# Kernel optimization log

Hardware: AMD Instinct MI355X
Metric: run time of the kernel (lower is better)

## Reference

```python
import jax, jax.numpy as jnp
import numpy as np

B, E, S, H = 8, 1024, 2048, 16  # batch, embed_dim, seq_len, n_heads
D = E // H                       # per-head hidden dim


def setup_inputs() -> dict:
    key = jax.random.key(0)
    k1, k2 = jax.random.split(key)
    x = jax.random.normal(k1, (B, E, S), dtype=jnp.float32)
    weight = jax.random.normal(k2, (H, S), dtype=jnp.float32)  # nn.Parameter(torch.randn)
    bias = jnp.zeros((H, S), dtype=jnp.float32)                # nn.Parameter(torch.zeros)
    return {"x": x, "weight": weight, "bias": bias}


def _vector_to_matrix(v):
    # v: (H, S) -> M: (H, S, S), M[h, i, j] = v[h, j - i] if j >= i else 0
    h, m = v.shape
    i = jnp.arange(m)[:, None]
    j = jnp.arange(m)[None, :]
    off = j - i  # negative offsets wrap (same as torch fancy indexing) but are masked out
    return jnp.where(j >= i, v[:, off], jnp.zeros((), dtype=v.dtype))


def reference(x, weight, bias):
    b, e, s = x.shape
    h = weight.shape[0]
    d = e // h
    M = _vector_to_matrix(weight)  # (H, S, S)
    # Original: x.view(B,H,D,S).reshape(B*H,D,S) paired with W.repeat_interleave(B,0),
    # i.e. flat index k uses M[k // B]. Group the flat B*H axis into H contiguous
    # blocks of size B so each block shares one Toeplitz matrix (no (B*H,S,S) blowup).
    xg = x.reshape(b * h, d, s).reshape(h, b, d, s)  # block m = M[m]
    out = jnp.einsum('mbds,mst->mbdt', xg, M) + bias[:, None, None, :]
    return out.reshape(b, e, s)
```

## Files before the change

### kernel.cpp

```cpp
#include <hip/hip_runtime.h>
#include <hip/hip_bf16.h>

#define SEQ    2048
#define NHEAD  16
#define RPH    512
#define BM     128
#define BK     64
#define NTH    256

#define WSTRIDE 2184
#define ABUF_E  8192
#define WCOP_E  (2 * ABUF_E)
#define TOT_E   (WCOP_E + 8 * WSTRIDE)

typedef float  f32x4  __attribute__((ext_vector_type(4)));
typedef __bf16 bf16x8 __attribute__((ext_vector_type(8)));

struct PF { float4 v0, v1, v2, v3, v4, v5, v6, v7; };

__device__ __forceinline__ unsigned f2bf(float f) {
    union { __hip_bfloat16 h; unsigned short u; } cv;
    cv.h = __float2bfloat16(f);
    return (unsigned)cv.u;
}

__device__ __forceinline__ uint4 pack8u(float4 a, float4 b) {
    union { bf16x8 v; uint4 u; } r;
    r.v[0] = (__bf16)a.x; r.v[1] = (__bf16)a.y;
    r.v[2] = (__bf16)a.z; r.v[3] = (__bf16)a.w;
    r.v[4] = (__bf16)b.x; r.v[5] = (__bf16)b.y;
    r.v[6] = (__bf16)b.z; r.v[7] = (__bf16)b.w;
    return r.u;
}

#define MFMA16(a, b, c) __builtin_amdgcn_mfma_f32_16x16x32_bf16((a), (b), (c), 0, 0, 0)

#define LOADPF(P, CH)                                                         \
  { const float* g_ = Xp + (size_t)(CH) * BK;                                 \
    P.v0 = *(const float4*)g_;                                                \
    P.v1 = *(const float4*)(g_ + 4);                                          \
    P.v2 = *(const float4*)(g_ + 8 * SEQ);                                    \
    P.v3 = *(const float4*)(g_ + 8 * SEQ + 4);                                \
    P.v4 = *(const float4*)(g_ + 16 * SEQ);                                   \
    P.v5 = *(const float4*)(g_ + 16 * SEQ + 4);                               \
    P.v6 = *(const float4*)(g_ + 24 * SEQ);                                   \
    P.v7 = *(const float4*)(g_ + 24 * SEQ + 4); }

#define WRITEA(AB, P)                                                         \
  { *(uint4*)((AB) + wb0) = pack8u(P.v0, P.v1);                               \
    *(uint4*)((AB) + wb1) = pack8u(P.v2, P.v3);                               \
    *(uint4*)((AB) + wb2) = pack8u(P.v4, P.v5);                               \
    *(uint4*)((AB) + wb3) = pack8u(P.v6, P.v7); }

#define WINLOAD4(CH, OFFE, S0, S1, S2, S3)                                    \
  { const unsigned short* bq_ = wcB + 64 * (CH) + (OFFE);                     \
    bw[S0] = *(const bf16x8*)(bq_);                                           \
    bw[S1] = *(const bf16x8*)(bq_ + 16);                                      \
    bw[S2] = *(const bf16x8*)(bq_ + 32);                                      \
    bw[S3] = *(const bf16x8*)(bq_ + 48); }

#define KSTEPW(ABC, KS, P8, BASE)                                             \
  { const int kb_ = (64 * (KS) + kq16) ^ swz;                                 \
    bf16x8 af0 = *(const bf16x8*)((ABC) + Arow0 + kb_);                       \
    bf16x8 af1 = *(const bf16x8*)((ABC) + Arow1 + kb_);                       \
    acc[0][0] = MFMA16(af0, bw[((P8)+(BASE)-0)&15], acc[0][0]);               \
    acc[1][0] = MFMA16(af1, bw[((P8)+(BASE)-0)&15], acc[1][0]);               \
    acc[0][1] = MFMA16(af0, bw[((P8)+(BASE)-1)&15], acc[0][1]);               \
    acc[1][1] = MFMA16(af1, bw[((P8)+(BASE)-1)&15], acc[1][1]);               \
    acc[0][2] = MFMA16(af0, bw[((P8)+(BASE)-2)&15], acc[0][2]);               \
    acc[1][2] = MFMA16(af1, bw[((P8)+(BASE)-2)&15], acc[1][2]);               \
    acc[0][3] = MFMA16(af0, bw[((P8)+(BASE)-3)&15], acc[0][3]);               \
    acc[1][3] = MFMA16(af1, bw[((P8)+(BASE)-3)&15], acc[1][3]);               \
    acc[0][4] = MFMA16(af0, bw[((P8)+(BASE)-4)&15], acc[0][4]);               \
    acc[1][4] = MFMA16(af1, bw[((P8)+(BASE)-4)&15], acc[1][4]);               \
    acc[0][5] = MFMA16(af0, bw[((P8)+(BASE)-5)&15], acc[0][5]);               \
    acc[1][5] = MFMA16(af1, bw[((P8)+(BASE)-5)&15], acc[1][5]);               \
    acc[0][6] = MFMA16(af0, bw[((P8)+(BASE)-6)&15], acc[0][6]);               \
    acc[1][6] = MFMA16(af1, bw[((P8)+(BASE)-6)&15], acc[1][6]);               \
    acc[0][7] = MFMA16(af0, bw[((P8)+(BASE)-7)&15], acc[0][7]);               \
    acc[1][7] = MFMA16(af1, bw[((P8)+(BASE)-7)&15], acc[1][7]); }

#define PAIRBODY(P8)                                                          \
  {                                                                           \
    if (ch + 2 < nch) LOADPF(pfA, ch + 2);                                    \
    WRITEA(ab1, pfB);                                                         \
    __builtin_amdgcn_s_setprio(1);                                            \
    KSTEPW(ab0, 0, P8, 7);                                                    \
    KSTEPW(ab0, 1, P8, 9);                                                    \
    __builtin_amdgcn_s_setprio(0);                                            \
    if (ch + 2 < nch)                                                         \
        WINLOAD4(ch, 112, ((P8)+14)&15, ((P8)+15)&15,                         \
                 ((P8)+16)&15, ((P8)+17)&15);                                 \
    if (ch + 3 < nch) LOADPF(pfB, ch + 3);                                    \
    if (ch + 2 < nch) WRITEA(ab0, pfA);                                       \
    __builtin_amdgcn_s_setprio(1);                                            \
    KSTEPW(ab1, 0, P8, 11);                                                   \
    KSTEPW(ab1, 1, P8, 13);                                                   \
    __builtin_amdgcn_s_setprio(0);                                            \
    if (ch + 2 < nch)                                                         \
        WINLOAD4(ch, 176, ((P8)+18)&15, ((P8)+19)&15,                         \
                 ((P8)+20)&15, ((P8)+21)&15);                                 \
  }

__global__ __launch_bounds__(NTH, 2) void mixer_kernel(
    const float* __restrict__ x, const float* __restrict__ wgt,
    const float* __restrict__ bias, float* __restrict__ out)
{
    __shared__ unsigned short smem[TOT_E] __attribute__((aligned(16)));
    char* ab0 = (char*)smem;
    char* ab1 = (char*)smem + ABUF_E * 2;
    unsigned short* wc = smem + WCOP_E;

    const int tid  = threadIdx.x;
    const int lane = tid & 63;
    const int wv   = tid >> 6;

    const int bid  = blockIdx.x;
    const int m    = (bid & 7) + 8 * ((bid >> 3) & 1);
    const int rt   = (bid >> 4) & 3;
    const int pr   = bid >> 6;
    const int ct_hi = 15 - pr;
    const int ct_lo = pr;

    const float* Xb = x   + (size_t)(m * RPH + rt * BM) * SEQ;
    float*       Ob = out + (size_t)(m * RPH + rt * BM) * SEQ;
    const float* wr = wgt  + m * SEQ;
    const float* br = bias + m * SEQ;

    const int sr    = lane >> 3;
    const int sc    = (lane & 7) * 8;
    const int wsw   = ((lane & 7) * 16) ^ (sr << 4);
    const int rbw   = 32 * wv;
    const int wb0   = (rbw + sr)      * 128 + wsw;
    const int wb1   = (rbw + sr + 8)  * 128 + wsw;
    const int wb2   = (rbw + sr + 16) * 128 + wsw;
    const int wb3   = (rbw + sr + 24) * 128 + wsw;
    const float* Xp = Xb + (size_t)(rbw + sr) * SEQ + sc;

    PF pfA, pfB;
    LOADPF(pfA, 0);
    LOADPF(pfB, 1);

    {
        const int t8 = tid * 8;
        const float* g = wr + (2040 - t8);
        float4 lo = *(const float4*)g;
        float4 hi = *(const float4*)(g + 4);
        uint4 v;
        v.x = f2bf(hi.w) | (f2bf(hi.z) << 16);
        v.y = f2bf(hi.y) | (f2bf(hi.x) << 16);
        v.z = f2bf(lo.w) | (f2bf(lo.z) << 16);
        v.w = f2bf(lo.y) | (f2bf(lo.x) << 16);
        *(uint4*)(smem + 8 + t8) = v;
        if (tid < 21) {
            uint4 z = {0u, 0u, 0u, 0u};
            unsigned short* dst = (tid == 0) ? smem
                                 : smem + 8 + 2048 + (tid - 1) * 8;
            *(uint4*)dst = z;
        }
    }
    __syncthreads();

    #pragma unroll
    for (int c = 0; c < 8; ++c) {
        for (int grp = tid; grp < WSTRIDE / 8; grp += NTH) {
            const int i = grp * 8;
            uint4 g0 = *(const uint4*)(smem + 8 + i - 8);
            uint4 g1 = *(const uint4*)(smem + 8 + i);
            unsigned d[9] = {g0.x, g0.y, g0.z, g0.w,
                             g1.x, g1.y, g1.z, g1.w, 0u};
            const int qd = (16 - 2 * c) >> 2;
            uint4 o;
            if (c & 1) {
                o.x = (d[qd]     >> 16) | (d[qd + 1] << 16);
                o.y = (d[qd + 1] >> 16) | (d[qd + 2] << 16);
                o.z = (d[qd + 2] >> 16) | (d[qd + 3] << 16);
                o.w = (d[qd + 3] >> 16) | (d[qd + 4] << 16);
            } else {
                o.x = d[qd];     o.y = d[qd + 1];
                o.z = d[qd + 2]; o.w = d[qd + 3];
            }
            *(uint4*)(wc + c * WSTRIDE + i) = o;
        }
    }
    __syncthreads();

    const int col_low = lane & 15;
    const int kq      = lane >> 4;
    const int kq16    = kq * 16;
    const int swz     = (col_low & 7) << 4;
    const int cpy     = (col_low + 1) & 7;
    const int BcBase  = cpy * WSTRIDE + cpy + 2047 - col_low + 8 * kq;
    const int Arow0   = (rbw      + col_low) * 128;
    const int Arow1   = (rbw + 16 + col_low) * 128;

    #pragma unroll
    for (int half = 0; half < 2; ++half) {
        const int ct  = half ? ct_lo : ct_hi;
        const int t0  = ct << 7;
        const int nch = 2 * (ct + 1);
        const unsigned short* wcB = wc + (BcBase - t0);

        if (half) { LOADPF(pfA, 0); LOADPF(pfB, 1); }
        WRITEA(ab0, pfA);

        bf16x8 bw[16];
        {
            const unsigned short* bq_ = wcB - 112;
            #pragma unroll
            for (int i = 0; i < 14; ++i)
                bw[i] = *(const bf16x8*)(bq_ + 16 * i);
        }

        f32x4 acc[2][8] = {};
        int ch = 0;
        for (;;) {
            PAIRBODY(0);
            ch += 2; if (ch >= nch) break;
            PAIRBODY(8);
            ch += 2; if (ch >= nch) break;
        }

        #pragma unroll
        for (int c = 0; c < 8; ++c) {
            const int colg = t0 + 16 * c + col_low;
            const float bv = br[colg];
            #pragma unroll
            for (int a = 0; a < 2; ++a) {
                const int rowl = rbw + 16 * a + 4 * kq;
                #pragma unroll
                for (int r = 0; r < 4; ++r)
                    Ob[(size_t)(rowl + r) * SEQ + colg] = acc[a][c][r] + bv;
            }
        }
    }
}

extern "C" void kernel_launch(void* const* d_in, const int* in_sizes, int n_in,
                              void* d_out, int out_size, void* d_ws, size_t ws_size,
                              hipStream_t stream) {
    const float* x  = (const float*)d_in[0];
    const float* w  = (const float*)d_in[1];
    const float* bs = (const float*)d_in[2];
    float* out = (float*)d_out;
    dim3 grid(512);
    dim3 block(NTH);
    hipLaunchKernelGGL(mixer_kernel, grid, block, 0, stream, x, w, bs, out);
}
```

Measured before the change: 46.07 us.

## Halve row tile and launch one column tile per block on a larger grid

```diff
diff --git a/kernel.cpp b/kernel.cpp
--- a/kernel.cpp
+++ b/kernel.cpp
@@ -4,19 +4,19 @@
 #define SEQ    2048
 #define NHEAD  16
 #define RPH    512
-#define BM     128
+#define BM     64
 #define BK     64
 #define NTH    256
 
 #define WSTRIDE 2184
-#define ABUF_E  8192
+#define ABUF_E  4096
 #define WCOP_E  (2 * ABUF_E)
 #define TOT_E   (WCOP_E + 8 * WSTRIDE)
 
 typedef float  f32x4  __attribute__((ext_vector_type(4)));
 typedef __bf16 bf16x8 __attribute__((ext_vector_type(8)));
 
-struct PF { float4 v0, v1, v2, v3, v4, v5, v6, v7; };
+struct PF { float4 v0, v1, v2, v3; };
 
 __device__ __forceinline__ unsigned f2bf(float f) {
     union { __hip_bfloat16 h; unsigned short u; } cv;
@@ -39,18 +39,12 @@
   { const float* g_ = Xp + (size_t)(CH) * BK;                                 \
     P.v0 = *(const float4*)g_;                                                \
     P.v1 = *(const float4*)(g_ + 4);                                          \
-    P.v2 = *(const float4*)(g_ + 8 * SEQ);                                    \
-    P.v3 = *(const float4*)(g_ + 8 * SEQ + 4);                                \
-    P.v4 = *(const float4*)(g_ + 16 * SEQ);                                   \
-    P.v5 = *(const float4*)(g_ + 16 * SEQ + 4);                               \
-    P.v6 = *(const float4*)(g_ + 24 * SEQ);                                   \
-    P.v7 = *(const float4*)(g_ + 24 * SEQ + 4); }
+    P.v2 = *(const float4*)(g_ + 8);                                          \
+    P.v3 = *(const float4*)(g_ + 12); }
 
 #define WRITEA(AB, P)                                                         \
   { *(uint4*)((AB) + wb0) = pack8u(P.v0, P.v1);                               \
-    *(uint4*)((AB) + wb1) = pack8u(P.v2, P.v3);                               \
-    *(uint4*)((AB) + wb2) = pack8u(P.v4, P.v5);                               \
-    *(uint4*)((AB) + wb3) = pack8u(P.v6, P.v7); }
+    *(uint4*)((AB) + wb1) = pack8u(P.v2, P.v3); }
 
 #define WINLOAD4(CH, OFFE, S0, S1, S2, S3)                                    \
   { const unsigned short* bq_ = wcB + 64 * (CH) + (OFFE);                     \
@@ -62,23 +56,14 @@
 #define KSTEPW(ABC, KS, P8, BASE)                                             \
   { const int kb_ = (64 * (KS) + kq16) ^ swz;                                 \
     bf16x8 af0 = *(const bf16x8*)((ABC) + Arow0 + kb_);                       \
-    bf16x8 af1 = *(const bf16x8*)((ABC) + Arow1 + kb_);                       \
-    acc[0][0] = MFMA16(af0, bw[((P8)+(BASE)-0)&15], acc[0][0]);               \
-    acc[1][0] = MFMA16(af1, bw[((P8)+(BASE)-0)&15], acc[1][0]);               \
-    acc[0][1] = MFMA16(af0, bw[((P8)+(BASE)-1)&15], acc[0][1]);               \
-    acc[1][1] = MFMA16(af1, bw[((P8)+(BASE)-1)&15], acc[1][1]);               \
-    acc[0][2] = MFMA16(af0, bw[((P8)+(BASE)-2)&15], acc[0][2]);               \
-    acc[1][2] = MFMA16(af1, bw[((P8)+(BASE)-2)&15], acc[1][2]);               \
-    acc[0][3] = MFMA16(af0, bw[((P8)+(BASE)-3)&15], acc[0][3]);               \
-    acc[1][3] = MFMA16(af1, bw[((P8)+(BASE)-3)&15], acc[1][3]);               \
-    acc[0][4] = MFMA16(af0, bw[((P8)+(BASE)-4)&15], acc[0][4]);               \
-    acc[1][4] = MFMA16(af1, bw[((P8)+(BASE)-4)&15], acc[1][4]);               \
-    acc[0][5] = MFMA16(af0, bw[((P8)+(BASE)-5)&15], acc[0][5]);               \
-    acc[1][5] = MFMA16(af1, bw[((P8)+(BASE)-5)&15], acc[1][5]);               \
-    acc[0][6] = MFMA16(af0, bw[((P8)+(BASE)-6)&15], acc[0][6]);               \
-    acc[1][6] = MFMA16(af1, bw[((P8)+(BASE)-6)&15], acc[1][6]);               \
-    acc[0][7] = MFMA16(af0, bw[((P8)+(BASE)-7)&15], acc[0][7]);               \
-    acc[1][7] = MFMA16(af1, bw[((P8)+(BASE)-7)&15], acc[1][7]); }
+    acc[0] = MFMA16(af0, bw[((P8)+(BASE)-0)&15], acc[0]);                     \
+    acc[1] = MFMA16(af0, bw[((P8)+(BASE)-1)&15], acc[1]);                     \
+    acc[2] = MFMA16(af0, bw[((P8)+(BASE)-2)&15], acc[2]);                     \
+    acc[3] = MFMA16(af0, bw[((P8)+(BASE)-3)&15], acc[3]);                     \
+    acc[4] = MFMA16(af0, bw[((P8)+(BASE)-4)&15], acc[4]);                     \
+    acc[5] = MFMA16(af0, bw[((P8)+(BASE)-5)&15], acc[5]);                     \
+    acc[6] = MFMA16(af0, bw[((P8)+(BASE)-6)&15], acc[6]);                     \
+    acc[7] = MFMA16(af0, bw[((P8)+(BASE)-7)&15], acc[7]); }
 
 #define PAIRBODY(P8)                                                          \
   {                                                                           \
@@ -102,7 +87,7 @@
                  ((P8)+20)&15, ((P8)+21)&15);                                 \
   }
 
-__global__ __launch_bounds__(NTH, 2) void mixer_kernel(
+__global__ __launch_bounds__(NTH, 3) void mixer_kernel(
     const float* __restrict__ x, const float* __restrict__ wgt,
     const float* __restrict__ bias, float* __restrict__ out)
 {
@@ -117,25 +102,22 @@
 
     const int bid  = blockIdx.x;
     const int m    = (bid & 7) + 8 * ((bid >> 3) & 1);
-    const int rt   = (bid >> 4) & 3;
-    const int pr   = bid >> 6;
-    const int ct_hi = 15 - pr;
-    const int ct_lo = pr;
+    const int rt   = (bid >> 4) & 7;
+    const int ct   = 15 - (bid >> 7);
+    const int t0   = ct << 7;
+    const int nch  = 2 * (ct + 1);
 
     const float* Xb = x   + (size_t)(m * RPH + rt * BM) * SEQ;
     float*       Ob = out + (size_t)(m * RPH + rt * BM) * SEQ;
     const float* wr = wgt  + m * SEQ;
     const float* br = bias + m * SEQ;
 
-    const int sr    = lane >> 3;
-    const int sc    = (lane & 7) * 8;
-    const int wsw   = ((lane & 7) * 16) ^ (sr << 4);
-    const int rbw   = 32 * wv;
-    const int wb0   = (rbw + sr)      * 128 + wsw;
-    const int wb1   = (rbw + sr + 8)  * 128 + wsw;
-    const int wb2   = (rbw + sr + 16) * 128 + wsw;
-    const int wb3   = (rbw + sr + 24) * 128 + wsw;
-    const float* Xp = Xb + (size_t)(rbw + sr) * SEQ + sc;
+    const int sr    = lane >> 2;
+    const int scq   = lane & 3;
+    const int rbw   = 16 * wv;
+    const int wb0   = (rbw + sr) * 128 + ((scq * 32) ^ ((sr & 7) << 4));
+    const int wb1   = (rbw + sr) * 128 + ((scq * 32 + 16) ^ ((sr & 7) << 4));
+    const float* Xp = Xb + (size_t)(rbw + sr) * SEQ + scq * 16;
 
     PF pfA, pfB;
     LOADPF(pfA, 0);
@@ -191,48 +173,36 @@
     const int swz     = (col_low & 7) << 4;
     const int cpy     = (col_low + 1) & 7;
     const int BcBase  = cpy * WSTRIDE + cpy + 2047 - col_low + 8 * kq;
-    const int Arow0   = (rbw      + col_low) * 128;
-    const int Arow1   = (rbw + 16 + col_low) * 128;
+    const int Arow0   = (rbw + col_low) * 128;
+    const unsigned short* wcB = wc + (BcBase - t0);
+
+    WRITEA(ab0, pfA);
+
+    bf16x8 bw[16];
+    {
+        const unsigned short* bq_ = wcB - 112;
+        #pragma unroll
+        for (int i = 0; i < 14; ++i)
+            bw[i] = *(const bf16x8*)(bq_ + 16 * i);
+    }
+
+    f32x4 acc[8] = {};
+    int ch = 0;
+    for (;;) {
+        PAIRBODY(0);
+        ch += 2; if (ch >= nch) break;
+        PAIRBODY(8);
+        ch += 2; if (ch >= nch) break;
+    }
 
     #pragma unroll
-    for (int half = 0; half < 2; ++half) {
-        const int ct  = half ? ct_lo : ct_hi;
-        const int t0  = ct << 7;
-        const int nch = 2 * (ct + 1);
-        const unsigned short* wcB = wc + (BcBase - t0);
-
-        if (half) { LOADPF(pfA, 0); LOADPF(pfB, 1); }
-        WRITEA(ab0, pfA);
-
-        bf16x8 bw[16];
-        {
-            const unsigned short* bq_ = wcB - 112;
-            #pragma unroll
-            for (int i = 0; i < 14; ++i)
-                bw[i] = *(const bf16x8*)(bq_ + 16 * i);
-        }
-
-        f32x4 acc[2][8] = {};
-        int ch = 0;
-        for (;;) {
-            PAIRBODY(0);
-            ch += 2; if (ch >= nch) break;
-            PAIRBODY(8);
-            ch += 2; if (ch >= nch) break;
-        }
-
+    for (int c = 0; c < 8; ++c) {
+        const int colg = t0 + 16 * c + col_low;
+        const float bv = br[colg];
+        const int rowl = rbw + 4 * kq;
         #pragma unroll
-        for (int c = 0; c < 8; ++c) {
-            const int colg = t0 + 16 * c + col_low;
-            const float bv = br[colg];
-            #pragma unroll
-            for (int a = 0; a < 2; ++a) {
-                const int rowl = rbw + 16 * a + 4 * kq;
-                #pragma unroll
-                for (int r = 0; r < 4; ++r)
-                    Ob[(size_t)(rowl + r) * SEQ + colg] = acc[a][c][r] + bv;
-            }
-        }
+        for (int r = 0; r < 4; ++r)
+            Ob[(size_t)(rowl + r) * SEQ + colg] = acc[c][r] + bv;
     }
 }
 
@@ -243,7 +213,7 @@
     const float* w  = (const float*)d_in[1];
     const float* bs = (const float*)d_in[2];
     float* out = (float*)d_out;
-    dim3 grid(512);
+    dim3 grid(2048);
     dim3 block(NTH);
     hipLaunchKernelGGL(mixer_kernel, grid, block, 0, stream, x, w, bs, out);
 }
```

Measured after the change: 80.68 us. +75.1%, slower.
